# Performance work log

Measured on AMD Instinct MI355X. Metric: run time of the kernel, lower is better.

Reference implementation:

```python
import jax, jax.numpy as jnp
import numpy as np

GRID_SIZE = 3
SPLINE_ORDER = 3
GRID_RANGE = (-1.0, 1.0)


def make_grid():
    # extended knot vector, shape (1, grid_size + 2*spline_order + 1) = (1, 10)
    h = (GRID_RANGE[1] - GRID_RANGE[0]) / GRID_SIZE
    pts = np.arange(-SPLINE_ORDER, GRID_SIZE + SPLINE_ORDER + 1, dtype=np.float32) * h + GRID_RANGE[0]
    return jnp.asarray(pts[None, :])  # broadcasts over in_features


def b_splines(x, grid):
    # x: (B, in) -> bases: (B, in, grid_size + spline_order)
    x = x[..., None]  # (B, in, 1)
    bases = ((x >= grid[:, :-1]) & (x < grid[:, 1:])).astype(x.dtype)
    for k in range(1, SPLINE_ORDER + 1):
        left = (x - grid[:, : -(k + 1)]) / (grid[:, k:-1] - grid[:, : -(k + 1)])
        right = (grid[:, k + 1:] - x) / (grid[:, k + 1:] - grid[:, 1:-k])
        bases = left * bases[..., :-1] + right * bases[..., 1:]
    return bases


def kan_linear(x, base_w, spline_w, scaler, grid):
    # efficient-kan KANLinear: silu(x)@base_w.T + b_splines(x) contracted with scaled spline weights
    base_out = jnp.einsum('bi,oi->bo', jax.nn.silu(x), base_w)
    bases = b_splines(x, grid)  # (B, in, 6)
    spline_out = jnp.einsum('bik,oik->bo', bases, spline_w * scaler[..., None])
    return base_out + spline_out


def layer_norm(x, gamma, beta, eps=1e-5):
    mu = jnp.mean(x, axis=-1, keepdims=True)
    var = jnp.mean(jnp.square(x - mu), axis=-1, keepdims=True)
    return (x - mu) * jax.lax.rsqrt(var + eps) * gamma + beta


def setup_inputs() -> dict:
    key = jax.random.key(0)
    ks = jax.random.split(key, 8)
    B, D_IN, D_HID, D_OUT = 16384, 1280, 512, 229
    NB = GRID_SIZE + SPLINE_ORDER  # 6 basis functions per input feature
    s1 = 1.0 / np.sqrt(D_IN)
    s2 = 1.0 / np.sqrt(D_HID)
    return {
        'x': jax.random.normal(ks[0], (B, D_IN), dtype=jnp.float32),
        'base_w1': jax.random.normal(ks[1], (D_HID, D_IN), dtype=jnp.float32) * s1,
        'spline_w1': jax.random.normal(ks[2], (D_HID, D_IN, NB), dtype=jnp.float32) * s1,
        'scaler1': jax.random.normal(ks[3], (D_HID, D_IN), dtype=jnp.float32) * 0.1 + 1.0,
        'ln_gamma': jnp.ones((D_HID,), dtype=jnp.float32),
        'ln_beta': jnp.zeros((D_HID,), dtype=jnp.float32),
        'base_w2': jax.random.normal(ks[4], (D_OUT, D_HID), dtype=jnp.float32) * s2,
        'spline_w2': jax.random.normal(ks[5], (D_OUT, D_HID, NB), dtype=jnp.float32) * s2,
        'scaler2': jax.random.normal(ks[6], (D_OUT, D_HID), dtype=jnp.float32) * 0.1 + 1.0,
    }


def reference(x, base_w1, spline_w1, scaler1, ln_gamma, ln_beta, base_w2, spline_w2, scaler2):
    grid = make_grid()
    h = kan_linear(x, base_w1, spline_w1, scaler1, grid)   # (B, 512)
    h = layer_norm(h, ln_gamma, ln_beta)                    # dropout: identity at inference
    out = kan_linear(h, base_w2, spline_w2, scaler2, grid)  # (B, 229)
    return out
```

## Files before the change

### kernel.cpp

```cpp
#include <hip/hip_runtime.h>


typedef short s16x8 __attribute__((ext_vector_type(8)));
typedef float f32x4 __attribute__((ext_vector_type(4)));

__device__ __forceinline__ void dma16(const void* g, void* l) {
  __builtin_amdgcn_global_load_lds(
      (const __attribute__((address_space(1))) unsigned int*)g,
      (__attribute__((address_space(3))) unsigned int*)l, 16, 0, 0);
}

template <int N>
__device__ __forceinline__ void wait_vm() {
  if constexpr (N == 0)      asm volatile("s_waitcnt vmcnt(0)" ::: "memory");
  else if constexpr (N == 5) asm volatile("s_waitcnt vmcnt(5)" ::: "memory");
  else if constexpr (N == 9) asm volatile("s_waitcnt vmcnt(9)" ::: "memory");
  else static_assert(N == 0, "unsupported vmcnt");
}

__device__ __forceinline__ unsigned pk2(float lo, float hi) {
  unsigned a = __float_as_uint(lo), b = __float_as_uint(hi);
  a = a + 0x7fffu + ((a >> 16) & 1u);
  b = b + 0x7fffu + ((b >> 16) & 1u);
  return __builtin_amdgcn_perm(b, a, 0x07060302u);
}

__device__ __forceinline__ unsigned short f2bf(float f) {
  unsigned u = __float_as_uint(f);
  unsigned r = u + 0x7fffu + ((u >> 16) & 1u);
  return (unsigned short)(r >> 16);
}

__device__ __forceinline__ uint4 kan_act8(float x) {
  float e = __expf(-x);
  float s = x * __builtin_amdgcn_rcpf(1.0f + e);
  float u = fmaf(x, 1.5f, 4.5f);
  float d[10];
#pragma unroll
  for (int j = 0; j < 10; ++j) d[j] = u - (float)j;
  float b1[8];
#pragma unroll
  for (int j = 0; j < 8; ++j) b1[j] = fmaxf(0.0f, 1.0f - fabsf(d[j + 1]));
  float B2[7];
#pragma unroll
  for (int j = 0; j < 7; ++j) B2[j] = d[j] * b1[j] - d[j + 3] * b1[j + 1];
  float b3[6];
#pragma unroll
  for (int j = 0; j < 6; ++j)
    b3[j] = (d[j] * B2[j] - d[j + 4] * B2[j + 1]) * (1.0f / 6.0f);
  uint4 r;
  r.x = pk2(s, b3[0]);
  r.y = pk2(b3[1], b3[2]);
  r.z = pk2(b3[3], b3[4]);
  r.w = pk2(b3[5], 0.0f);
  return r;
}

__global__ __launch_bounds__(256) void prep_w(
    const float* __restrict__ base_w, const float* __restrict__ spline_w,
    const float* __restrict__ scaler, short* __restrict__ Wp,
    int F, int Nvalid) {
  int i = blockIdx.x * 256 + threadIdx.x;
  int n = blockIdx.y;
  if (i >= F) return;
  s16x8 v;
#pragma unroll
  for (int k = 0; k < 8; ++k) v[k] = 0;
  if (n < Nvalid) {
    int idx = n * F + i;
    float sc = scaler[idx];
    v[0] = (short)f2bf(base_w[idx]);
#pragma unroll
    for (int k = 0; k < 6; ++k) v[1 + k] = (short)f2bf(spline_w[idx * 6 + k] * sc);
  }
  int p = (i & ~3) | ((i & 3) ^ (n & 3));
  *(s16x8*)&Wp[((size_t)n * F + p) * 8] = v;
}

template <int BN>
__global__ __launch_bounds__(256, 2) void kan_gemm(
    const float* __restrict__ X, const short* __restrict__ W,
    float* __restrict__ Cp, int F, int span, long long pstride,
    int ldc, int ncols) {
  constexpr int NT = BN / 64;
  constexpr int IE = BN / 64;
  __shared__ __align__(16) short As[2][64 * 32];
  __shared__ __align__(16) short Bs[2][BN * 32];

  const int t    = threadIdx.x;
  const int lane = t & 63;
  const int w    = t >> 6;
  const int m0   = blockIdx.x * 64;
  const int f0   = blockIdx.z * span;

  const int wcol = w * (BN / 4);
  const int mrow = lane & 15;
  const int q    = lane >> 4;
  const int qs   = (q ^ (mrow & 3)) * 8;

  int a_off[4], b_off[NT];
#pragma unroll
  for (int it = 0; it < 4; ++it)
    a_off[it] = (it * 16 + mrow) * 32 + qs;
#pragma unroll
  for (int jt = 0; jt < NT; ++jt)
    b_off[jt] = (wcol + jt * 16 + mrow) * 32 + qs;

  const int sr = t >> 2, sj = t & 3;
  const float* xq = X + (size_t)(m0 + sr) * F + f0 + sj;
  const int aw = sr * 32 + ((sj ^ (sr & 3)) * 8);

  const int drow = w * (BN / 4) + (lane >> 2);
  const int dchk = lane & 3;
  const char* wg = (const char*)W + ((size_t)drow * F + f0 + dchk) * 16;
  const size_t gistr = (size_t)16 * F * 16;

  f32x4 acc[4][NT] = {};
  const int nsteps = span >> 2;

  float x0 = *xq;
#pragma unroll
  for (int e = 0; e < IE; ++e)
    dma16(wg + e * gistr, &Bs[0][(w * (BN / 4) + e * 16) * 32]);
  {
    uint4 av = kan_act8(x0);
    *(uint4*)&As[0][aw] = av;
  }
  float xA = (nsteps > 1) ? xq[4] : 0.0f;
  __syncthreads();

  for (int ks = 0; ks < nsteps; ++ks) {
    const int cb = ks & 1, nb = cb ^ 1;
    const bool more = (ks + 1 < nsteps);

    float xB = 0.0f;
    if (ks + 2 < nsteps) xB = xq[(size_t)(ks + 2) * 4];

    if (more) {
#pragma unroll
      for (int e = 0; e < IE; ++e)
        dma16(wg + (size_t)(ks + 1) * 64 + e * gistr,
              &Bs[nb][(w * (BN / 4) + e * 16) * 32]);
      wait_vm<IE + 1>();
    } else {
      wait_vm<0>();
    }

    s16x8 af[4], bfr[NT];
#pragma unroll
    for (int it = 0; it < 4; ++it)
      af[it] = *(const s16x8*)&As[cb][a_off[it]];
#pragma unroll
    for (int jt = 0; jt < NT; ++jt)
      bfr[jt] = *(const s16x8*)&Bs[cb][b_off[jt]];
    __builtin_amdgcn_s_setprio(1);
#pragma unroll
    for (int b = 0; b < NT; ++b)
#pragma unroll
      for (int a = 0; a < 4; ++a)
        acc[a][b] = __builtin_amdgcn_mfma_f32_16x16x32_bf16(
            af[a], bfr[b], acc[a][b], 0, 0, 0);
    __builtin_amdgcn_s_setprio(0);

    if (more) {
      uint4 av = kan_act8(xA);
      *(uint4*)&As[nb][aw] = av;
      xA = xB;
    }
    asm volatile("s_waitcnt lgkmcnt(0)" ::: "memory");
    __builtin_amdgcn_s_barrier();
  }

  float* cpt = Cp + (size_t)blockIdx.z * (size_t)pstride;
#pragma unroll
  for (int a = 0; a < 4; ++a) {
#pragma unroll
    for (int b = 0; b < NT; ++b) {
      int col = wcol + b * 16 + mrow;
      if (col < ncols) {
#pragma unroll
        for (int r = 0; r < 4; ++r) {
          int row = m0 + a * 16 + q * 4 + r;
          cpt[(size_t)row * ldc + col] = acc[a][b][r];
        }
      }
    }
  }
}

__global__ __launch_bounds__(256) void ln_reduce(
    const float* __restrict__ p0, const float* __restrict__ p1,
    float* __restrict__ h, const float* __restrict__ gamma,
    const float* __restrict__ beta, int nparts) {
  int lane = threadIdx.x & 63;
  int wv   = threadIdx.x >> 6;
  int row  = blockIdx.x * 4 + wv;
  size_t base = (size_t)row * 512 + lane * 8;
  f32x4 v0 = *(const f32x4*)(p0 + base);
  f32x4 v1 = *(const f32x4*)(p0 + base + 4);
  if (nparts == 2) {
    f32x4 u0 = *(const f32x4*)(p1 + base);
    f32x4 u1 = *(const f32x4*)(p1 + base + 4);
#pragma unroll
    for (int k = 0; k < 4; ++k) { v0[k] += u0[k]; v1[k] += u1[k]; }
  }
  float s = 0.f, s2 = 0.f;
#pragma unroll
  for (int k = 0; k < 4; ++k) { s += v0[k] + v1[k]; s2 += v0[k]*v0[k] + v1[k]*v1[k]; }
#pragma unroll
  for (int m = 32; m >= 1; m >>= 1) {
    s  += __shfl_xor(s,  m, 64);
    s2 += __shfl_xor(s2, m, 64);
  }
  float mean = s * (1.0f / 512.0f);
  float var  = s2 * (1.0f / 512.0f) - mean * mean;
  float rstd = rsqrtf(var + 1e-5f);
  const f32x4 g0 = *(const f32x4*)(gamma + lane * 8);
  const f32x4 g1 = *(const f32x4*)(gamma + lane * 8 + 4);
  const f32x4 be0 = *(const f32x4*)(beta + lane * 8);
  const f32x4 be1 = *(const f32x4*)(beta + lane * 8 + 4);
#pragma unroll
  for (int k = 0; k < 4; ++k) {
    v0[k] = (v0[k] - mean) * rstd * g0[k] + be0[k];
    v1[k] = (v1[k] - mean) * rstd * g1[k] + be1[k];
  }
  *(f32x4*)(h + base) = v0;
  *(f32x4*)(h + base + 4) = v1;
}

__global__ __launch_bounds__(256) void out_reduce(
    const float* __restrict__ p0, const float* __restrict__ p1,
    float* __restrict__ out, int nparts) {
  int idx = blockIdx.x * 256 + threadIdx.x;
  int row = idx >> 8;
  int c   = idx & 255;
  float v = p0[idx];
  if (nparts == 2) v += p1[idx];
  if (c < 229) out[(size_t)row * 229 + c] = v;
}

extern "C" void kernel_launch(void* const* d_in, const int* in_sizes, int n_in,
                              void* d_out, int out_size, void* d_ws, size_t ws_size,
                              hipStream_t stream) {
  const float* x         = (const float*)d_in[0];
  const float* base_w1   = (const float*)d_in[1];
  const float* spline_w1 = (const float*)d_in[2];
  const float* scaler1   = (const float*)d_in[3];
  const float* ln_gamma  = (const float*)d_in[4];
  const float* ln_beta   = (const float*)d_in[5];
  const float* base_w2   = (const float*)d_in[6];
  const float* spline_w2 = (const float*)d_in[7];
  const float* scaler2   = (const float*)d_in[8];
  float* out = (float*)d_out;

  const int B = 16384, D_IN = 1280, D_HID = 512, D_OUT = 229;

  const size_t szW1 = (size_t)D_HID * D_IN * 8 * 2;
  const size_t szW2 = (size_t)256 * D_HID * 8 * 2;
  const size_t szH  = (size_t)B * D_HID * 4;
  const size_t szP  = (size_t)B * 512 * 4;
  char* ws = (char*)d_ws;
  short* W1p = (short*)ws;
  short* W2p = (short*)(ws + szW1);
  float* h   = (float*)(ws + szW1 + szW2);
  float* p0  = (float*)(ws + szW1 + szW2 + szH);
  float* p1  = (float*)(ws + szW1 + szW2 + szH + szP);

  const int parts = (ws_size >= szW1 + szW2 + szH + 2 * szP) ? 2 : 1;
  const long long pstride = (long long)(szP / 4);

  prep_w<<<dim3(D_IN / 256, D_HID), 256, 0, stream>>>(
      base_w1, spline_w1, scaler1, W1p, D_IN, D_HID);
  prep_w<<<dim3(D_HID / 256, 256), 256, 0, stream>>>(
      base_w2, spline_w2, scaler2, W2p, D_HID, D_OUT);

  kan_gemm<512><<<dim3(B / 64, 1, parts), 256, 0, stream>>>(
      x, W1p, p0, D_IN, D_IN / parts, pstride, D_HID, D_HID);

  ln_reduce<<<dim3(B / 4), 256, 0, stream>>>(p0, p1, h, ln_gamma, ln_beta, parts);

  kan_gemm<256><<<dim3(B / 64, 1, parts), 256, 0, stream>>>(
      h, W2p, p0, D_HID, D_HID / parts, pstride, 256, 256);

  out_reduce<<<dim3(B * 256 / 256), 256, 0, stream>>>(p0, p1, out, parts);
}
```

Before: 454.0 us.

## Split first KAN GEMM into 256-column tiles and raise occupancy to 4 blocks

The first-layer GEMM now uses BN=256 tiles with a second grid dimension over output columns instead of one 512-wide tile per block. Launch bounds rise from 2 to 4 blocks per CU, which cuts register use and shared memory per block and doubles the block count. The s_setprio calls around the MFMA loop are removed, and LDS offsets are computed from one base plus immediates to free registers. The cost is that the A tile (the activation expansion of x) is now recomputed and reloaded by two blocks per row tile.

```diff
diff --git a/kernel.cpp b/kernel.cpp
--- a/kernel.cpp
+++ b/kernel.cpp
@@ -78,7 +78,7 @@
 }
 
 template <int BN>
-__global__ __launch_bounds__(256, 2) void kan_gemm(
+__global__ __launch_bounds__(256, 4) void kan_gemm(
     const float* __restrict__ X, const short* __restrict__ W,
     float* __restrict__ Cp, int F, int span, long long pstride,
     int ldc, int ncols) {
@@ -91,6 +91,7 @@
   const int lane = t & 63;
   const int w    = t >> 6;
   const int m0   = blockIdx.x * 64;
+  const int c0   = blockIdx.y * BN;
   const int f0   = blockIdx.z * span;
 
   const int wcol = w * (BN / 4);
@@ -98,19 +99,14 @@
   const int q    = lane >> 4;
   const int qs   = (q ^ (mrow & 3)) * 8;
 
-  int a_off[4], b_off[NT];
-#pragma unroll
-  for (int it = 0; it < 4; ++it)
-    a_off[it] = (it * 16 + mrow) * 32 + qs;
-#pragma unroll
-  for (int jt = 0; jt < NT; ++jt)
-    b_off[jt] = (wcol + jt * 16 + mrow) * 32 + qs;
+  const int a_lo = mrow * 32 + qs;
+  const int b_lo = (wcol + mrow) * 32 + qs;
 
   const int sr = t >> 2, sj = t & 3;
   const float* xq = X + (size_t)(m0 + sr) * F + f0 + sj;
   const int aw = sr * 32 + ((sj ^ (sr & 3)) * 8);
 
-  const int drow = w * (BN / 4) + (lane >> 2);
+  const int drow = c0 + wcol + (lane >> 2);
   const int dchk = lane & 3;
   const char* wg = (const char*)W + ((size_t)drow * F + f0 + dchk) * 16;
   const size_t gistr = (size_t)16 * F * 16;
@@ -121,7 +117,7 @@
   float x0 = *xq;
 #pragma unroll
   for (int e = 0; e < IE; ++e)
-    dma16(wg + e * gistr, &Bs[0][(w * (BN / 4) + e * 16) * 32]);
+    dma16(wg + e * gistr, &Bs[0][(wcol + e * 16) * 32]);
   {
     uint4 av = kan_act8(x0);
     *(uint4*)&As[0][aw] = av;
@@ -140,27 +136,27 @@
 #pragma unroll
       for (int e = 0; e < IE; ++e)
         dma16(wg + (size_t)(ks + 1) * 64 + e * gistr,
-              &Bs[nb][(w * (BN / 4) + e * 16) * 32]);
+              &Bs[nb][(wcol + e * 16) * 32]);
       wait_vm<IE + 1>();
     } else {
       wait_vm<0>();
     }
 
+    const short* Ac = As[cb];
+    const short* Bc = Bs[cb];
     s16x8 af[4], bfr[NT];
 #pragma unroll
     for (int it = 0; it < 4; ++it)
-      af[it] = *(const s16x8*)&As[cb][a_off[it]];
+      af[it] = *(const s16x8*)(Ac + a_lo + it * (16 * 32));
 #pragma unroll
     for (int jt = 0; jt < NT; ++jt)
-      bfr[jt] = *(const s16x8*)&Bs[cb][b_off[jt]];
-    __builtin_amdgcn_s_setprio(1);
+      bfr[jt] = *(const s16x8*)(Bc + b_lo + jt * (16 * 32));
 #pragma unroll
     for (int b = 0; b < NT; ++b)
 #pragma unroll
       for (int a = 0; a < 4; ++a)
         acc[a][b] = __builtin_amdgcn_mfma_f32_16x16x32_bf16(
             af[a], bfr[b], acc[a][b], 0, 0, 0);
-    __builtin_amdgcn_s_setprio(0);
 
     if (more) {
       uint4 av = kan_act8(xA);
@@ -176,11 +172,11 @@
   for (int a = 0; a < 4; ++a) {
 #pragma unroll
     for (int b = 0; b < NT; ++b) {
-      int col = wcol + b * 16 + mrow;
+      int col = c0 + wcol + b * 16 + mrow;
       if (col < ncols) {
 #pragma unroll
         for (int r = 0; r < 4; ++r) {
-          int row = m0 + a * 16 + q * 4 + r;
+          int row = m0 + a * 16 + (lane >> 4) * 4 + r;
           cpt[(size_t)row * ldc + col] = acc[a][b][r];
         }
       }
@@ -274,7 +270,7 @@
   prep_w<<<dim3(D_HID / 256, 256), 256, 0, stream>>>(
       base_w2, spline_w2, scaler2, W2p, D_HID, D_OUT);
 
-  kan_gemm<512><<<dim3(B / 64, 1, parts), 256, 0, stream>>>(
+  kan_gemm<256><<<dim3(B / 64, D_HID / 256, parts), 256, 0, stream>>>(
       x, W1p, p0, D_IN, D_IN / parts, pstride, D_HID, D_HID);
 
   ln_reduce<<<dim3(B / 4), 256, 0, stream>>>(p0, p1, h, ln_gamma, ln_beta, parts);
```

Result: slower. 466.8 us (+2.8%).
